# Kernel tuning notes

Hardware: AMD Instinct MI355X
Metric: run time of the kernel (lower is better)

Reference implementation:

```python
import jax, jax.numpy as jnp
import numpy as np

N_NODES = 100000
N_EDGES = 3200000
D_IN, D_HID, D_OUT = 512, 256, 64


def setup_inputs() -> dict:
    key = jax.random.key(0)
    ks = jax.random.split(key, 8)
    x = jax.random.normal(ks[0], (N_NODES, D_IN), dtype=jnp.float32)
    row = jax.random.randint(ks[1], (N_EDGES,), 0, N_NODES, dtype=jnp.int64)
    col = jax.random.randint(ks[2], (N_EDGES,), 0, N_NODES, dtype=jnp.int64)
    edge_weight = jax.random.uniform(ks[3], (N_EDGES,), dtype=jnp.float32)
    w1 = jax.random.normal(ks[4], (D_IN, D_HID), dtype=jnp.float32) * (1.0 / np.sqrt(D_HID))
    b1 = jax.random.normal(ks[5], (D_HID,), dtype=jnp.float32) * (1.0 / np.sqrt(D_HID))
    w2 = jax.random.normal(ks[6], (D_HID, D_OUT), dtype=jnp.float32) * (1.0 / np.sqrt(D_OUT))
    b2 = jax.random.normal(ks[7], (D_OUT,), dtype=jnp.float32) * (1.0 / np.sqrt(D_OUT))
    return {"x": x, "row": row, "col": col, "edge_weight": edge_weight,
            "w1": w1, "b1": b1, "w2": w2, "b2": b2}


def _gc_layer(h, row, col, edge_weight, w, b, n_nodes):
    # support = h @ w ; out = spmm(adj, support) + b
    support = h @ w                                   # [N, d_out]
    msgs = edge_weight[:, None] * support[col]        # gather source rows
    agg = jax.ops.segment_sum(msgs, row, num_segments=n_nodes)
    return agg + b


def reference(x, row, col, edge_weight, w1, b1, w2, b2):
    n = x.shape[0]
    h = jax.nn.relu(_gc_layer(x, row, col, edge_weight, w1, b1, n))
    # dropout p=0.0 -> identity
    h = _gc_layer(h, row, col, edge_weight, w2, b2, n)
    return jax.nn.log_softmax(h, axis=1)
```

## Files before the change

### kernel.cpp

```cpp
#include <hip/hip_runtime.h>
#include <hip/hip_bf16.h>
#include <hip/hip_fp8.h>

#define N_NODES 100000
#define N_EDGES 3200000
#define D_IN 512
#define D_HID 256
#define D_OUT 64
#define M_PAD 100096

#define NB 782
#define EPB 8192
#define NBLK_BIN ((N_EDGES + EPB - 1) / EPB)

typedef __attribute__((ext_vector_type(8))) short bf16x8;
typedef __attribute__((ext_vector_type(4))) float f32x4;

__device__ __forceinline__ unsigned short f2bf(float f) {
    __hip_bfloat16 h = __float2bfloat16(f);
    return *reinterpret_cast<unsigned short*>(&h);
}
__device__ __forceinline__ float f8f(unsigned int byte) {
    __hip_fp8_e4m3 t;
    t.__x = (__hip_fp8_storage_t)byte;
    return (float)t;
}


__global__ void cast_w1t_kernel(const float* __restrict__ w1, __hip_bfloat16* __restrict__ w1t) {
    int i = blockIdx.x * 256 + threadIdx.x;
    if (i >= D_IN * D_HID) return;
    int k = i / D_HID, n = i % D_HID;
    w1t[n * D_IN + k] = __float2bfloat16(w1[i]);
}

__global__ void cast_w2t_kernel(const float* __restrict__ w2, __hip_bfloat16* __restrict__ w2t) {
    int i = blockIdx.x * 256 + threadIdx.x;
    if (i >= D_HID * D_OUT) return;
    int k = i / D_OUT, n = i % D_OUT;
    w2t[n * D_HID + k] = __float2bfloat16(w2[i]);
}


__global__ __launch_bounds__(256) void hist_bucket_kernel(const int* __restrict__ row,
                                                          int* __restrict__ gcnt) {
    __shared__ int cnt[NB];
    for (int i = threadIdx.x; i < NB; i += 256) cnt[i] = 0;
    __syncthreads();
    int base = blockIdx.x * EPB;
    for (int i = threadIdx.x; i < EPB; i += 256) {
        int e = base + i;
        if (e < N_EDGES) atomicAdd(&cnt[row[e] >> 7], 1);
    }
    __syncthreads();
    for (int i = threadIdx.x; i < NB; i += 256) {
        int c = cnt[i];
        if (c) atomicAdd(&gcnt[i], c);
    }
}

__global__ void scan_nb_kernel(const int* __restrict__ gcnt, int* __restrict__ boff,
                               int* __restrict__ gcur, int* __restrict__ offsets) {
    __shared__ int smem[1024];
    int t = threadIdx.x;
    int v = (t < NB) ? gcnt[t] : 0;
    smem[t] = v;
    __syncthreads();
    for (int off = 1; off < 1024; off <<= 1) {
        int u = (t >= off) ? smem[t - off] : 0;
        __syncthreads();
        smem[t] += u;
        __syncthreads();
    }
    int excl = smem[t] - v;
    if (t < NB) { boff[t] = excl; gcur[t] = excl; }
    if (t == 1023) boff[NB] = smem[1023];
    if (t == 0) offsets[N_NODES] = N_EDGES;
}

__global__ __launch_bounds__(256) void bin_kernel(const int* __restrict__ row,
                                                  const int* __restrict__ col,
                                                  const float* __restrict__ ew,
                                                  int* __restrict__ gcur,
                                                  int2* __restrict__ bucketed) {
    __shared__ int cnt[NB];
    __shared__ int cur[NB];
    for (int i = threadIdx.x; i < NB; i += 256) cnt[i] = 0;
    __syncthreads();
    int base = blockIdx.x * EPB;
    for (int i = threadIdx.x; i < EPB; i += 256) {
        int e = base + i;
        if (e < N_EDGES) atomicAdd(&cnt[row[e] >> 7], 1);
    }
    __syncthreads();
    for (int i = threadIdx.x; i < NB; i += 256) {
        int c = cnt[i];
        cur[i] = c ? atomicAdd(&gcur[i], c) : 0;
    }
    __syncthreads();
    for (int i = threadIdx.x; i < EPB; i += 256) {
        int e = base + i;
        if (e < N_EDGES) {
            int r = row[e];
            int b = r >> 7;
            int pos = atomicAdd(&cur[b], 1);
            bucketed[pos] = make_int2((col[e] << 7) | (r & 127), __float_as_int(ew[e]));
        }
    }
}

__global__ __launch_bounds__(256) void csr_kernel(const int2* __restrict__ bucketed,
                                                  const int* __restrict__ boff,
                                                  int* __restrict__ offsets,
                                                  int2* __restrict__ edges) {
    __shared__ int rcnt[128];
    __shared__ int sc[128];
    __shared__ int rcur[128];
    int b = blockIdx.x;
    int t = threadIdx.x;
    int s = boff[b], e2 = boff[b + 1];
    if (t < 128) rcnt[t] = 0;
    __syncthreads();
    for (int i = s + t; i < e2; i += 256) atomicAdd(&rcnt[bucketed[i].x & 127], 1);
    __syncthreads();
    if (t < 128) sc[t] = rcnt[t];
    __syncthreads();
    for (int off = 1; off < 128; off <<= 1) {
        int u = 0;
        if (t < 128 && t >= off) u = sc[t - off];
        __syncthreads();
        if (t < 128) sc[t] += u;
        __syncthreads();
    }
    if (t < 128) {
        int excl = sc[t] - rcnt[t];
        rcur[t] = excl;
        int rglob = b * 128 + t;
        if (rglob < N_NODES) offsets[rglob] = s + excl;
    }
    __syncthreads();
    for (int i = s + t; i < e2; i += 256) {
        int2 p = bucketed[i];
        int r = p.x & 127;
        int pos = atomicAdd(&rcur[r], 1);
        edges[s + pos] = make_int2(p.x >> 7, p.y);
    }
}


template <int BN, int WROWS, int WCOLS, int MT, int NT, bool A_F32, int OUT_MODE>
__global__ __launch_bounds__(256) void gemm_bf16_kernel(
    const void* __restrict__ Av, const __hip_bfloat16* __restrict__ Bt,
    void* __restrict__ Cv, int K, int Mvalid, int Nld) {
    constexpr int BM = 128;
    constexpr int BK = 32;
    constexpr int LDT = BK + 8;
    __shared__ __align__(16) __hip_bfloat16 As[BM][LDT];
    __shared__ __align__(16) __hip_bfloat16 Bs[BN][LDT];

    const int tid = threadIdx.x;
    const int m0 = blockIdx.x * BM;
    const int n0 = blockIdx.y * BN;
    const int w = tid >> 6, lane = tid & 63;
    const int wr = w % WROWS, wc = w / WROWS;
    const int mbase = wr * MT * 16, nbase = wc * NT * 16;
    const int quad = lane >> 4, l16 = lane & 15;

    f32x4 acc[MT][NT] = {};

    constexpr int ACH = (BM * BK) / (256 * 8);
    constexpr int BCH = (BN * BK) / (256 * 8);

    for (int k0 = 0; k0 < K; k0 += BK) {
#pragma unroll
        for (int c = 0; c < ACH; ++c) {
            int idx = (tid + c * 256) * 8;
            int r = idx / BK, kk = idx % BK;
            if constexpr (A_F32) {
                int grow = m0 + r;
                uint4 o;
                if (grow < Mvalid) {
                    const float* ap = (const float*)Av + (size_t)grow * K + k0 + kk;
                    float4 f0 = *reinterpret_cast<const float4*>(ap);
                    float4 f1 = *reinterpret_cast<const float4*>(ap + 4);
                    o.x = (unsigned)f2bf(f0.x) | ((unsigned)f2bf(f0.y) << 16);
                    o.y = (unsigned)f2bf(f0.z) | ((unsigned)f2bf(f0.w) << 16);
                    o.z = (unsigned)f2bf(f1.x) | ((unsigned)f2bf(f1.y) << 16);
                    o.w = (unsigned)f2bf(f1.z) | ((unsigned)f2bf(f1.w) << 16);
                } else {
                    o = uint4{0, 0, 0, 0};
                }
                *reinterpret_cast<uint4*>(&As[r][kk]) = o;
            } else {
                *reinterpret_cast<uint4*>(&As[r][kk]) = *reinterpret_cast<const uint4*>(
                    (const __hip_bfloat16*)Av + (size_t)(m0 + r) * K + k0 + kk);
            }
        }
#pragma unroll
        for (int c = 0; c < BCH; ++c) {
            int idx = (tid + c * 256) * 8;
            int r = idx / BK, kk = idx % BK;
            *reinterpret_cast<uint4*>(&Bs[r][kk]) =
                *reinterpret_cast<const uint4*>(&Bt[(size_t)(n0 + r) * K + k0 + kk]);
        }
        __syncthreads();

        bf16x8 af[MT], bfr[NT];
#pragma unroll
        for (int mt = 0; mt < MT; ++mt)
            af[mt] = *reinterpret_cast<bf16x8*>(&As[mbase + mt * 16 + l16][quad * 8]);
#pragma unroll
        for (int nt = 0; nt < NT; ++nt)
            bfr[nt] = *reinterpret_cast<bf16x8*>(&Bs[nbase + nt * 16 + l16][quad * 8]);
#pragma unroll
        for (int mt = 0; mt < MT; ++mt)
#pragma unroll
            for (int nt = 0; nt < NT; ++nt)
                acc[mt][nt] = __builtin_amdgcn_mfma_f32_16x16x32_bf16(af[mt], bfr[nt],
                                                                      acc[mt][nt], 0, 0, 0);
        __syncthreads();
    }

#pragma unroll
    for (int mt = 0; mt < MT; ++mt)
#pragma unroll
        for (int nt = 0; nt < NT; ++nt)
#pragma unroll
            for (int r = 0; r < 4; ++r) {
                int rowi = m0 + mbase + mt * 16 + quad * 4 + r;
                int coli = n0 + nbase + nt * 16 + l16;
                if (rowi < Mvalid) {
                    if constexpr (OUT_MODE == 0) {
                        ((float*)Cv)[(size_t)rowi * Nld + coli] = acc[mt][nt][r];
                    } else if constexpr (OUT_MODE == 1) {
                        ((__hip_bfloat16*)Cv)[(size_t)rowi * Nld + coli] =
                            __float2bfloat16(acc[mt][nt][r]);
                    } else {
                        __hip_fp8_e4m3 q(acc[mt][nt][r]);
                        ((unsigned char*)Cv)[(size_t)rowi * Nld + coli] = q.__x;
                    }
                }
            }
}


__global__ __launch_bounds__(256) void agg1_kernel(
    const unsigned int* __restrict__ sup,
    const int* __restrict__ offsets, const int2* __restrict__ edges,
    const float* __restrict__ b1, __hip_bfloat16* __restrict__ hb) {
    int n = blockIdx.x * 4 + (threadIdx.x >> 6);
    int lane = threadIdx.x & 63;
    if (n >= M_PAD) return;
    if (n >= N_NODES) {
        *reinterpret_cast<ushort4*>(&hb[(size_t)n * D_HID + lane * 4]) = ushort4{0, 0, 0, 0};
        return;
    }
    int s = offsets[n], e2 = offsets[n + 1];
    float a0 = 0.f, a1 = 0.f, a2 = 0.f, a3 = 0.f;
    int e = s;
    for (; e + 8 <= e2; e += 8) {
        int2 m[8];
        unsigned int v[8];
#pragma unroll
        for (int i = 0; i < 8; ++i) m[i] = edges[e + i];
#pragma unroll
        for (int i = 0; i < 8; ++i) v[i] = sup[(size_t)m[i].x * 64 + lane];
#pragma unroll
        for (int i = 0; i < 8; ++i) {
            float wv = __int_as_float(m[i].y);
            a0 += wv * f8f(v[i] & 0xff);
            a1 += wv * f8f((v[i] >> 8) & 0xff);
            a2 += wv * f8f((v[i] >> 16) & 0xff);
            a3 += wv * f8f(v[i] >> 24);
        }
    }
    for (; e < e2; ++e) {
        int2 m = edges[e];
        unsigned int v = sup[(size_t)m.x * 64 + lane];
        float wv = __int_as_float(m.y);
        a0 += wv * f8f(v & 0xff);
        a1 += wv * f8f((v >> 8) & 0xff);
        a2 += wv * f8f((v >> 16) & 0xff);
        a3 += wv * f8f(v >> 24);
    }
    float4 bb = reinterpret_cast<const float4*>(b1)[lane];
    ushort4 o;
    o.x = f2bf(fmaxf(a0 + bb.x, 0.f));
    o.y = f2bf(fmaxf(a1 + bb.y, 0.f));
    o.z = f2bf(fmaxf(a2 + bb.z, 0.f));
    o.w = f2bf(fmaxf(a3 + bb.w, 0.f));
    *reinterpret_cast<ushort4*>(&hb[(size_t)n * D_HID + lane * 4]) = o;
}

__global__ __launch_bounds__(256) void agg2_softmax_kernel(
    const unsigned short* __restrict__ sup2, const int* __restrict__ offsets,
    const int2* __restrict__ edges, const float* __restrict__ b2, float* __restrict__ out) {
    int n = blockIdx.x * 4 + (threadIdx.x >> 6);
    int j = threadIdx.x & 63;
    if (n >= N_NODES) return;
    int s = offsets[n], e2 = offsets[n + 1];
    float acc = 0.f;
    int e = s;
    for (; e + 4 <= e2; e += 4) {
        int2 m0 = edges[e], m1 = edges[e + 1], m2 = edges[e + 2], m3 = edges[e + 3];
        float v0 = __uint_as_float((unsigned)sup2[(size_t)m0.x * D_OUT + j] << 16);
        float v1 = __uint_as_float((unsigned)sup2[(size_t)m1.x * D_OUT + j] << 16);
        float v2 = __uint_as_float((unsigned)sup2[(size_t)m2.x * D_OUT + j] << 16);
        float v3 = __uint_as_float((unsigned)sup2[(size_t)m3.x * D_OUT + j] << 16);
        acc += __int_as_float(m0.y) * v0;
        acc += __int_as_float(m1.y) * v1;
        acc += __int_as_float(m2.y) * v2;
        acc += __int_as_float(m3.y) * v3;
    }
    for (; e < e2; ++e) {
        int2 m = edges[e];
        acc += __int_as_float(m.y) * __uint_as_float((unsigned)sup2[(size_t)m.x * D_OUT + j] << 16);
    }
    acc += b2[j];
    float m = acc;
#pragma unroll
    for (int o = 32; o > 0; o >>= 1) m = fmaxf(m, __shfl_xor(m, o, 64));
    float ex = __expf(acc - m);
    float ssum = ex;
#pragma unroll
    for (int o = 32; o > 0; o >>= 1) ssum += __shfl_xor(ssum, o, 64);
    out[(size_t)n * D_OUT + j] = acc - m - __logf(ssum);
}


extern "C" void kernel_launch(void* const* d_in, const int* in_sizes, int n_in,
                              void* d_out, int out_size, void* d_ws, size_t ws_size,
                              hipStream_t stream) {
    const float* x  = (const float*)d_in[0];
    const int* row  = (const int*)d_in[1];
    const int* col  = (const int*)d_in[2];
    const float* ew = (const float*)d_in[3];
    const float* w1 = (const float*)d_in[4];
    const float* b1 = (const float*)d_in[5];
    const float* w2 = (const float*)d_in[6];
    const float* b2 = (const float*)d_in[7];
    float* out = (float*)d_out;

    char* ws = (char*)d_ws;
    size_t off = 0;
    auto alloc = [&](size_t bytes) -> void* {
        void* p = ws + off;
        off = (off + bytes + 255) & ~(size_t)255;
        return p;
    };

    __hip_bfloat16* w1t  = (__hip_bfloat16*)alloc((size_t)D_HID * D_IN * 2);
    __hip_bfloat16* w2t  = (__hip_bfloat16*)alloc((size_t)D_OUT * D_HID * 2);
    unsigned char* sup1  = (unsigned char*)alloc((size_t)N_NODES * D_HID);
    __hip_bfloat16* hb   = (__hip_bfloat16*)alloc((size_t)M_PAD * D_HID * 2);
    unsigned short* sup2 = (unsigned short*)alloc((size_t)N_NODES * D_OUT * 2);
    int* offsets         = (int*)alloc((size_t)(N_NODES + 1) * 4);
    int* gcnt            = (int*)alloc((size_t)NB * 4);
    int* boff            = (int*)alloc((size_t)(NB + 1) * 4);
    int* gcur            = (int*)alloc((size_t)NB * 4);
    int2* edges          = (int2*)alloc((size_t)N_EDGES * 8);
    int2* bucketed       = (int2*)alloc((size_t)N_EDGES * 8);

    hipMemsetAsync(gcnt, 0, (size_t)NB * 4, stream);
    hist_bucket_kernel<<<NBLK_BIN, 256, 0, stream>>>(row, gcnt);
    scan_nb_kernel<<<1, 1024, 0, stream>>>(gcnt, boff, gcur, offsets);
    bin_kernel<<<NBLK_BIN, 256, 0, stream>>>(row, col, ew, gcur, bucketed);
    csr_kernel<<<NB, 256, 0, stream>>>(bucketed, boff, offsets, edges);

    cast_w1t_kernel<<<(D_IN * D_HID + 255) / 256, 256, 0, stream>>>(w1, w1t);
    cast_w2t_kernel<<<(D_HID * D_OUT + 255) / 256, 256, 0, stream>>>(w2, w2t);

    gemm_bf16_kernel<128, 2, 2, 4, 4, true, 2><<<dim3(M_PAD / 128, D_HID / 128), 256, 0, stream>>>(
        x, w1t, sup1, D_IN, N_NODES, D_HID);
    agg1_kernel<<<M_PAD / 4, 256, 0, stream>>>((const unsigned int*)sup1, offsets, edges, b1, hb);

    gemm_bf16_kernel<64, 4, 1, 2, 4, false, 1><<<dim3(M_PAD / 128, 1), 256, 0, stream>>>(
        hb, w2t, sup2, D_HID, N_NODES, D_OUT);
    agg2_softmax_kernel<<<(N_NODES + 3) / 4, 256, 0, stream>>>(sup2, offsets, edges, b2, out);
}
```

Measured before the change: 770.3 us.

## Prefetch next GEMM K-tile into registers while computing current tile

```diff
diff --git a/kernel.cpp b/kernel.cpp
--- a/kernel.cpp
+++ b/kernel.cpp
@@ -171,28 +171,27 @@
     constexpr int ACH = (BM * BK) / (256 * 8);
     constexpr int BCH = (BN * BK) / (256 * 8);
 
-    for (int k0 = 0; k0 < K; k0 += BK) {
+    float4 a0[ACH], a1[ACH];
+    uint4 ar[ACH];
+    uint4 br[BCH];
+
+    auto load_tile = [&](int k0) {
 #pragma unroll
         for (int c = 0; c < ACH; ++c) {
             int idx = (tid + c * 256) * 8;
             int r = idx / BK, kk = idx % BK;
             if constexpr (A_F32) {
                 int grow = m0 + r;
-                uint4 o;
                 if (grow < Mvalid) {
                     const float* ap = (const float*)Av + (size_t)grow * K + k0 + kk;
-                    float4 f0 = *reinterpret_cast<const float4*>(ap);
-                    float4 f1 = *reinterpret_cast<const float4*>(ap + 4);
-                    o.x = (unsigned)f2bf(f0.x) | ((unsigned)f2bf(f0.y) << 16);
-                    o.y = (unsigned)f2bf(f0.z) | ((unsigned)f2bf(f0.w) << 16);
-                    o.z = (unsigned)f2bf(f1.x) | ((unsigned)f2bf(f1.y) << 16);
-                    o.w = (unsigned)f2bf(f1.z) | ((unsigned)f2bf(f1.w) << 16);
+                    a0[c] = *reinterpret_cast<const float4*>(ap);
+                    a1[c] = *reinterpret_cast<const float4*>(ap + 4);
                 } else {
-                    o = uint4{0, 0, 0, 0};
+                    a0[c] = float4{0.f, 0.f, 0.f, 0.f};
+                    a1[c] = float4{0.f, 0.f, 0.f, 0.f};
                 }
-                *reinterpret_cast<uint4*>(&As[r][kk]) = o;
             } else {
-                *reinterpret_cast<uint4*>(&As[r][kk]) = *reinterpret_cast<const uint4*>(
+                ar[c] = *reinterpret_cast<const uint4*>(
                     (const __hip_bfloat16*)Av + (size_t)(m0 + r) * K + k0 + kk);
             }
         }
@@ -200,9 +199,40 @@
         for (int c = 0; c < BCH; ++c) {
             int idx = (tid + c * 256) * 8;
             int r = idx / BK, kk = idx % BK;
-            *reinterpret_cast<uint4*>(&Bs[r][kk]) =
-                *reinterpret_cast<const uint4*>(&Bt[(size_t)(n0 + r) * K + k0 + kk]);
-        }
+            br[c] = *reinterpret_cast<const uint4*>(&Bt[(size_t)(n0 + r) * K + k0 + kk]);
+        }
+    };
+
+    auto store_tile = [&]() {
+#pragma unroll
+        for (int c = 0; c < ACH; ++c) {
+            int idx = (tid + c * 256) * 8;
+            int r = idx / BK, kk = idx % BK;
+            if constexpr (A_F32) {
+                uint4 o;
+                o.x = (unsigned)f2bf(a0[c].x) | ((unsigned)f2bf(a0[c].y) << 16);
+                o.y = (unsigned)f2bf(a0[c].z) | ((unsigned)f2bf(a0[c].w) << 16);
+                o.z = (unsigned)f2bf(a1[c].x) | ((unsigned)f2bf(a1[c].y) << 16);
+                o.w = (unsigned)f2bf(a1[c].z) | ((unsigned)f2bf(a1[c].w) << 16);
+                *reinterpret_cast<uint4*>(&As[r][kk]) = o;
+            } else {
+                *reinterpret_cast<uint4*>(&As[r][kk]) = ar[c];
+            }
+        }
+#pragma unroll
+        for (int c = 0; c < BCH; ++c) {
+            int idx = (tid + c * 256) * 8;
+            int r = idx / BK, kk = idx % BK;
+            *reinterpret_cast<uint4*>(&Bs[r][kk]) = br[c];
+        }
+    };
+
+    load_tile(0);
+    const int NK = K / BK;
+    for (int it = 0; it < NK; ++it) {
+        if (it > 0) __syncthreads();
+        store_tile();
+        if (it + 1 < NK) load_tile((it + 1) * BK);
         __syncthreads();
 
         bf16x8 af[MT], bfr[NT];
@@ -218,7 +248,6 @@
             for (int nt = 0; nt < NT; ++nt)
                 acc[mt][nt] = __builtin_amdgcn_mfma_f32_16x16x32_bf16(af[mt], bfr[nt],
                                                                       acc[mt][nt], 0, 0, 0);
-        __syncthreads();
     }
 
 #pragma unroll
```

Result: slower. 795.2 us (+3.2%).
